# Kernel optimization log

Hardware: AMD Instinct MI355X
Metric: run time of the kernel (lower is better)

## Reference

```python
import jax, jax.numpy as jnp
import numpy as np

# 5-point Laplacian stencil (OIHW), scaled by 1/h^2 = N^2 at each level
FIXED = jnp.array([[[[0.0, 1.0, 0.0], [1.0, -4.0, 1.0], [0.0, 1.0, 0.0]]]], dtype=jnp.float32)
# flex_cycle schedule: depth-2 V-cycle, weighted Jacobi (smoother==1) everywhere
INTERGRID = [-1, -1, 0, 1, 1]
WEIGHT = [0.8, 0.8, 0.8, 0.8, 0.8]
N_GRID = 4096


def _conv(x, k, stride=1):
    return jax.lax.conv_general_dilated(x, k, (stride, stride), 'VALID',
                                        dimension_numbers=('NCHW', 'OIHW', 'NCHW'))


def _pad1(x):
    return jnp.pad(x, ((0, 0), (0, 0), (1, 1), (1, 1)))


def _apply_A(u):
    # F.conv2d(u, N^2 * stencil, padding=0) then zero-pad back to full size
    n = u.shape[-1]
    return _pad1(_conv(u, float(n * n) * FIXED))


def _jacobi(u, f, omega):
    # trainable_weight == 0 and trainable_stencil == fixed_stencil, so the
    # torch update collapses to standard weighted Jacobi
    n = u.shape[-1]
    central = -4.0 * float(n * n)
    return u + omega * (f - _apply_A(u)) / central


def _restrict(r, R):
    return _conv(r, R, stride=2)


def _prolong(u, P):
    up = jnp.repeat(jnp.repeat(u, 2, axis=2), 2, axis=3)  # nearest x2
    return _pad1(_conv(up, P))


def _vcycle(f, R, P):
    u = jnp.zeros_like(f)
    us, fs, lvl = [u], [f], 0
    for op, w in zip(INTERGRID, WEIGHT):
        if op == -1:  # smooth, restrict residual
            us[lvl] = _jacobi(us[lvl], fs[lvl], w)
            r = fs[lvl] - _apply_A(us[lvl])
            fs.append(_restrict(r, R))
            us.append(jnp.zeros_like(fs[-1]))
            lvl += 1
        elif op == 1:  # prolongate + correct, then smooth
            us[lvl - 1] = us[lvl - 1] + _prolong(us[lvl], P)
            lvl -= 1
            us[lvl] = _jacobi(us[lvl], fs[lvl], w)
        else:  # smooth in place
            us[lvl] = _jacobi(us[lvl], fs[lvl], w)
    return us[0]


def setup_inputs() -> dict:
    key = jax.random.key(0)
    f = jax.random.normal(key, (1, 1, N_GRID, N_GRID), dtype=jnp.float32)
    R = jnp.full((1, 1, 2, 2), 0.25, dtype=jnp.float32)
    P = jnp.array([[[[0.25, 0.5, 0.25], [0.5, 1.0, 0.5], [0.25, 0.5, 0.25]]]], dtype=jnp.float32)
    return {"f": f, "restriction_stencils": R, "prolongation_stencils": P}


def reference(f, restriction_stencils, prolongation_stencils):
    # forward() sets max_iter=1 and initial residual (u=0) is 1 > tol,
    # so exactly one flex_cycle runs
    u = _vcycle(f, restriction_stencils, prolongation_stencils)
    res = jnp.sum(jnp.abs(f - _apply_A(u))) / jnp.sum(jnp.abs(f))
    return (u, res)
```

## Files before the change

kernel.cpp:

```cpp
#include <hip/hip_runtime.h>

#define N0 4096
#define N1 2048
#define N2 1024

__global__ __launch_bounds__(256, 4) void k_res_restrict(const float* __restrict__ f,
                                                         float* __restrict__ fc,
                                                         int n, int nc) {
    const int tid = threadIdx.x;
    const int tx = tid & 63, ty = tid >> 6;
    const int fy0 = blockIdx.y * 16, fx0 = blockIdx.x * 256;
    const bool laneL = (tx == 0), laneR = (tx == 63);
    const bool edge = (blockIdx.x == 0) | (blockIdx.y == 0) |
                      (blockIdx.x == gridDim.x - 1) | (blockIdx.y == gridDim.y - 1);

    float4 o4[6]; float os[6];
    #pragma unroll
    for (int rr = 0; rr < 6; ++rr) {
        int gy = max(0, min(n - 1, fy0 + 4 * ty - 1 + rr));
        const float* rowp = f + (size_t)gy * n;
        o4[rr] = *(const float4*)(rowp + fx0 + 4 * tx);
        if (laneL) os[rr] = rowp[max(0, fx0 - 1)];
        if (laneR) os[rr] = rowp[min(n - 1, fx0 + 256)];
    }
    float fa[6][6];
    #pragma unroll
    for (int rr = 0; rr < 6; ++rr) {
        fa[rr][1] = o4[rr].x; fa[rr][2] = o4[rr].y; fa[rr][3] = o4[rr].z; fa[rr][4] = o4[rr].w;
        fa[rr][0] = __shfl_up(o4[rr].w, 1);
        fa[rr][5] = __shfl_down(o4[rr].x, 1);
        if (laneL) fa[rr][0] = os[rr];
        if (laneR) fa[rr][5] = os[rr];
    }
    float rv[4][4];
    #pragma unroll
    for (int i = 0; i < 4; ++i) {
        #pragma unroll
        for (int j = 0; j < 4; ++j) {
            float c = fa[1 + i][1 + j];
            rv[i][j] = c + 0.2f * (fa[i][1 + j] + fa[2 + i][1 + j] +
                                   fa[1 + i][j] + fa[1 + i][2 + j] - 4.0f * c);
        }
    }
    if (edge) {
        #pragma unroll
        for (int i = 0; i < 4; ++i)
            #pragma unroll
            for (int j = 0; j < 4; ++j) {
                int gy = fy0 + 4 * ty + i, gx = fx0 + 4 * tx + j;
                if (gy == 0 || gy == n - 1 || gx == 0 || gx == n - 1)
                    rv[i][j] = fa[1 + i][1 + j];
            }
    }
    #pragma unroll
    for (int da = 0; da < 2; ++da) {
        float2 o;
        o.x = 0.25f * (rv[2*da][0] + rv[2*da][1] + rv[2*da+1][0] + rv[2*da+1][1]);
        o.y = 0.25f * (rv[2*da][2] + rv[2*da][3] + rv[2*da+1][2] + rv[2*da+1][3]);
        *(float2*)(fc + (size_t)(fy0 / 2 + 2 * ty + da) * nc + (fx0 / 2 + 2 * tx)) = o;
    }
}

template <bool RESID>
__global__ __launch_bounds__(512, 4) void k_smooth_wide(
        const float* __restrict__ f, const float* __restrict__ uc,
        float* __restrict__ u, int n, int m, float cf, float cs,
        double* __restrict__ pT, double* __restrict__ pF) {
    __shared__ __align__(16) float su[RESID ? 18 : 1][260];
    __shared__ double sred[16];
    const int tid = threadIdx.x;
    const int tx = tid & 63, ty = tid >> 6;
    const int bx0 = blockIdx.x * 256, by0 = blockIdx.y * 16;
    const int Y  = by0 + 2 * ty;
    const int A0 = by0 >> 1;
    const int A  = A0 + ty;
    const int C  = (bx0 >> 1) + 2 * tx;
    const bool laneL = (tx == 0), laneR = (tx == 63);
    const bool edge = (blockIdx.x == 0) | (blockIdx.y == 0) |
                      (blockIdx.x == gridDim.x - 1) | (blockIdx.y == gridDim.y - 1);

    float4 f4[4]; float fs[4];
    #pragma unroll
    for (int r = 0; r < 4; ++r) {
        int gy = max(0, min(n - 1, Y - 1 + r));
        const float* rowp = f + (size_t)gy * n;
        f4[r] = *(const float4*)(rowp + bx0 + 4 * tx);
        if (laneL) fs[r] = rowp[max(0, bx0 - 1)];
        if (laneR) fs[r] = rowp[min(n - 1, bx0 + 256)];
    }
    float2 c2[3]; float csd[3];
    #pragma unroll
    for (int i = 0; i < 3; ++i) {
        int ga = max(0, min(m - 1, A - 1 + i));
        const float* cp = uc + (size_t)ga * m;
        c2[i] = *(const float2*)(cp + C);
        if (laneL) csd[i] = cp[max(0, C - 1)];
        if (laneR) csd[i] = cp[min(m - 1, C + 2)];
    }
    float4 fH4 = make_float4(0.f, 0.f, 0.f, 0.f); float fHs = 0.f;
    float2 cH2 = make_float2(0.f, 0.f);            float cHs = 0.f;
    float fsd2[2] = {0.f, 0.f}; float csd2[3] = {0.f, 0.f, 0.f};
    if (RESID) {
        if (ty == 0) {
            const float* rowp = f + (size_t)max(0, by0 - 2) * n;
            fH4 = *(const float4*)(rowp + bx0 + 4 * tx);
            if (laneL) fHs = rowp[max(0, bx0 - 1)];
            if (laneR) fHs = rowp[min(n - 1, bx0 + 256)];
            const float* cp = uc + (size_t)max(0, A0 - 2) * m;
            cH2 = *(const float2*)(cp + C);
            if (laneL) cHs = cp[max(0, C - 1)];
            if (laneR) cHs = cp[min(m - 1, C + 2)];
        }
        if (ty == 7) {
            const float* rowp = f + (size_t)min(n - 1, by0 + 17) * n;
            fH4 = *(const float4*)(rowp + bx0 + 4 * tx);
            if (laneL) fHs = rowp[max(0, bx0 - 1)];
            if (laneR) fHs = rowp[min(n - 1, bx0 + 256)];
            const float* cp = uc + (size_t)min(m - 1, A0 + 9) * m;
            cH2 = *(const float2*)(cp + C);
            if (laneL) cHs = cp[max(0, C - 1)];
            if (laneR) cHs = cp[min(m - 1, C + 2)];
        }
        if (laneL) {
            #pragma unroll
            for (int i = 0; i < 3; ++i) {
                int ga = max(0, min(m - 1, A - 1 + i));
                csd2[i] = uc[(size_t)ga * m + max(0, C - 2)];
            }
            #pragma unroll
            for (int k = 0; k < 2; ++k)
                fsd2[k] = f[(size_t)(Y + k) * n + max(0, bx0 - 2)];
        }
        if (laneR) {
            #pragma unroll
            for (int i = 0; i < 3; ++i) {
                int ga = max(0, min(m - 1, A - 1 + i));
                csd2[i] = uc[(size_t)ga * m + min(m - 1, C + 3)];
            }
            #pragma unroll
            for (int k = 0; k < 2; ++k)
                fsd2[k] = f[(size_t)(Y + k) * n + min(n - 1, bx0 + 257)];
        }
    }

    float fr[4][6];
    #pragma unroll
    for (int r = 0; r < 4; ++r) {
        fr[r][1] = f4[r].x; fr[r][2] = f4[r].y; fr[r][3] = f4[r].z; fr[r][4] = f4[r].w;
        fr[r][0] = __shfl_up(f4[r].w, 1);
        fr[r][5] = __shfl_down(f4[r].x, 1);
        if (laneL) fr[r][0] = fs[r];
        if (laneR) fr[r][5] = fs[r];
    }
    float cu[3][4];
    #pragma unroll
    for (int i = 0; i < 3; ++i) {
        float l  = __shfl_up(c2[i].y, 1);
        float rg = __shfl_down(c2[i].x, 1);
        if (laneL) l  = csd[i];
        if (laneR) rg = csd[i];
        cu[i][0] = cs * l; cu[i][1] = cs * c2[i].x; cu[i][2] = cs * c2[i].y; cu[i][3] = cs * rg;
    }
    float h[3][6];
    #pragma unroll
    for (int i = 0; i < 3; ++i) {
        h[i][0] = 1.5f * cu[i][0] + 0.5f * cu[i][1];
        h[i][1] = 0.5f * cu[i][0] + 1.5f * cu[i][1];
        h[i][2] = 1.5f * cu[i][1] + 0.5f * cu[i][2];
        h[i][3] = 0.5f * cu[i][1] + 1.5f * cu[i][2];
        h[i][4] = 1.5f * cu[i][2] + 0.5f * cu[i][3];
        h[i][5] = 0.5f * cu[i][2] + 1.5f * cu[i][3];
    }
    float v[4][6];
    #pragma unroll
    for (int j = 0; j < 6; ++j) {
        v[0][j] = 1.5f * h[0][j] + 0.5f * h[1][j] + cf * fr[0][j];
        v[1][j] = 0.5f * h[0][j] + 1.5f * h[1][j] + cf * fr[1][j];
        v[2][j] = 1.5f * h[1][j] + 0.5f * h[2][j] + cf * fr[2][j];
        v[3][j] = 0.5f * h[1][j] + 1.5f * h[2][j] + cf * fr[3][j];
    }
    if (edge) {
        #pragma unroll
        for (int r = 0; r < 4; ++r)
            #pragma unroll
            for (int j = 0; j < 6; ++j) {
                int gy = Y - 1 + r, gx = bx0 + 4 * tx - 1 + j;
                if (gy == 0 || gy == n - 1 || gx == 0 || gx == n - 1) v[r][j] = cf * fr[r][j];
            }
    }
    float u2[2][4];
    #pragma unroll
    for (int rr = 0; rr < 2; ++rr)
        #pragma unroll
        for (int cc = 0; cc < 4; ++cc) {
            float vc = v[1 + rr][1 + cc];
            u2[rr][cc] = vc + cf * fr[1 + rr][1 + cc]
                       + 0.2f * (v[rr][1 + cc] + v[2 + rr][1 + cc] +
                                 v[1 + rr][cc] + v[1 + rr][2 + cc] - 4.0f * vc);
        }
    if (edge) {
        #pragma unroll
        for (int rr = 0; rr < 2; ++rr)
            #pragma unroll
            for (int cc = 0; cc < 4; ++cc) {
                int gy = Y + rr, gx = bx0 + 4 * tx + cc;
                if (gy == 0 || gy == n - 1 || gx == 0 || gx == n - 1)
                    u2[rr][cc] = v[1 + rr][1 + cc] + cf * fr[1 + rr][1 + cc];
            }
    }
    #pragma unroll
    for (int rr = 0; rr < 2; ++rr)
        *(float4*)(u + (size_t)(Y + rr) * n + (bx0 + 4 * tx)) =
            make_float4(u2[rr][0], u2[rr][1], u2[rr][2], u2[rr][3]);

    if (RESID) {
        if (ty == 0) {
            float l  = __shfl_up(cH2.y, 1);
            float rg = __shfl_down(cH2.x, 1);
            if (laneL) l  = cHs;
            if (laneR) rg = cHs;
            l *= cs; rg *= cs;
            float ox = cs * cH2.x, oy = cs * cH2.y;
            float hm[4] = { 0.5f * l + 1.5f * ox, 1.5f * ox + 0.5f * oy,
                            0.5f * ox + 1.5f * oy, 1.5f * oy + 0.5f * rg };
            float fmv[4] = { fH4.x, fH4.y, fH4.z, fH4.w };
            float vm[4], uHt[4];
            #pragma unroll
            for (int cc = 0; cc < 4; ++cc) vm[cc] = 0.5f * hm[cc] + 1.5f * h[0][1 + cc] + cf * fmv[cc];
            if (edge) {
                #pragma unroll
                for (int cc = 0; cc < 4; ++cc) {
                    int gx = bx0 + 4 * tx + cc;
                    if (gx == 0 || gx == n - 1) vm[cc] = cf * fmv[cc];
                }
            }
            #pragma unroll
            for (int cc = 0; cc < 4; ++cc) {
                float vc = v[0][1 + cc];
                uHt[cc] = vc + cf * fr[0][1 + cc]
                        + 0.2f * (vm[cc] + v[1][1 + cc] + v[0][cc] + v[0][2 + cc] - 4.0f * vc);
            }
            if (edge) {
                #pragma unroll
                for (int cc = 0; cc < 4; ++cc) {
                    int gx = bx0 + 4 * tx + cc;
                    if (gx == 0 || gx == n - 1) uHt[cc] = v[0][1 + cc] + cf * fr[0][1 + cc];
                }
            }
            *(float4*)&su[0][4 * tx] = make_float4(uHt[0], uHt[1], uHt[2], uHt[3]);
        }
        if (ty == 7) {
            float l  = __shfl_up(cH2.y, 1);
            float rg = __shfl_down(cH2.x, 1);
            if (laneL) l  = cHs;
            if (laneR) rg = cHs;
            l *= cs; rg *= cs;
            float ox = cs * cH2.x, oy = cs * cH2.y;
            float hp[4] = { 0.5f * l + 1.5f * ox, 1.5f * ox + 0.5f * oy,
                            0.5f * ox + 1.5f * oy, 1.5f * oy + 0.5f * rg };
            float fpv[4] = { fH4.x, fH4.y, fH4.z, fH4.w };
            float vp[4], uHb[4];
            #pragma unroll
            for (int cc = 0; cc < 4; ++cc) vp[cc] = 1.5f * h[2][1 + cc] + 0.5f * hp[cc] + cf * fpv[cc];
            if (edge) {
                #pragma unroll
                for (int cc = 0; cc < 4; ++cc) {
                    int gx = bx0 + 4 * tx + cc;
                    if (gx == 0 || gx == n - 1) vp[cc] = cf * fpv[cc];
                }
            }
            #pragma unroll
            for (int cc = 0; cc < 4; ++cc) {
                float vc = v[3][1 + cc];
                uHb[cc] = vc + cf * fr[3][1 + cc]
                        + 0.2f * (v[2][1 + cc] + vp[cc] + v[3][cc] + v[3][2 + cc] - 4.0f * vc);
            }
            if (edge) {
                #pragma unroll
                for (int cc = 0; cc < 4; ++cc) {
                    int gx = bx0 + 4 * tx + cc;
                    if (gx == 0 || gx == n - 1) uHb[cc] = v[3][1 + cc] + cf * fr[3][1 + cc];
                }
            }
            *(float4*)&su[17][4 * tx] = make_float4(uHb[0], uHb[1], uHb[2], uHb[3]);
        }
        float uL[2] = {0.f, 0.f}, uR[2] = {0.f, 0.f};
        if (laneL) {
            float hL[3];
            #pragma unroll
            for (int i = 0; i < 3; ++i) hL[i] = 0.5f * cs * csd2[i] + 1.5f * cu[i][0];
            float vL[2] = { 0.5f * hL[0] + 1.5f * hL[1] + cf * fsd2[0],
                            1.5f * hL[1] + 0.5f * hL[2] + cf * fsd2[1] };
            if (edge) {
                #pragma unroll
                for (int k = 0; k < 2; ++k) {
                    int gy = Y + k;
                    if (gy == 0 || gy == n - 1) vL[k] = cf * fsd2[k];
                }
            }
            #pragma unroll
            for (int rr = 0; rr < 2; ++rr) {
                float vc = v[1 + rr][0];
                uL[rr] = vc + cf * fr[1 + rr][0]
                       + 0.2f * (v[rr][0] + v[2 + rr][0] + vL[rr] + v[1 + rr][1] - 4.0f * vc);
                if (edge) {
                    int gy = Y + rr;
                    if (gy == 0 || gy == n - 1) uL[rr] = vc + cf * fr[1 + rr][0];
                }
            }
        }
        if (laneR) {
            float hR[3];
            #pragma unroll
            for (int i = 0; i < 3; ++i) hR[i] = 1.5f * cu[i][3] + 0.5f * cs * csd2[i];
            float vR[2] = { 0.5f * hR[0] + 1.5f * hR[1] + cf * fsd2[0],
                            1.5f * hR[1] + 0.5f * hR[2] + cf * fsd2[1] };
            if (edge) {
                #pragma unroll
                for (int k = 0; k < 2; ++k) {
                    int gy = Y + k;
                    if (gy == 0 || gy == n - 1) vR[k] = cf * fsd2[k];
                }
            }
            #pragma unroll
            for (int rr = 0; rr < 2; ++rr) {
                float vc = v[1 + rr][5];
                uR[rr] = vc + cf * fr[1 + rr][5]
                       + 0.2f * (v[rr][5] + v[2 + rr][5] + v[1 + rr][4] + vR[rr] - 4.0f * vc);
                if (edge) {
                    int gy = Y + rr;
                    if (gy == 0 || gy == n - 1) uR[rr] = vc + cf * fr[1 + rr][5];
                }
            }
        }
        #pragma unroll
        for (int rr = 0; rr < 2; ++rr)
            *(float4*)&su[2 * ty + 1 + rr][4 * tx] =
                make_float4(u2[rr][0], u2[rr][1], u2[rr][2], u2[rr][3]);
        __syncthreads();
        float4 tv = *(const float4*)&su[2 * ty][4 * tx];
        float4 bv = *(const float4*)&su[2 * ty + 3][4 * tx];
        float ta[4] = { tv.x, tv.y, tv.z, tv.w };
        float ba[4] = { bv.x, bv.y, bv.z, bv.w };
        float lft[2], rgt[2];
        lft[0] = __shfl_up(u2[0][3], 1);   lft[1] = __shfl_up(u2[1][3], 1);
        rgt[0] = __shfl_down(u2[0][0], 1); rgt[1] = __shfl_down(u2[1][0], 1);
        if (laneL) { lft[0] = uL[0]; lft[1] = uL[1]; }
        if (laneR) { rgt[0] = uR[0]; rgt[1] = uR[1]; }
        const float n2 = (float)n * (float)n;
        float accT = 0.0f, accF = 0.0f;
        #pragma unroll
        for (int rr = 0; rr < 2; ++rr)
            #pragma unroll
            for (int cc = 0; cc < 4; ++cc) {
                float up = (rr == 0) ? ta[cc] : u2[0][cc];
                float dn = (rr == 1) ? ba[cc] : u2[1][cc];
                float lf = (cc == 0) ? lft[rr] : u2[rr][cc - 1];
                float rt = (cc == 3) ? rgt[rr] : u2[rr][cc + 1];
                float uu = u2[rr][cc];
                float fij = fr[1 + rr][1 + cc];
                float L = up + dn + lf + rt - 4.0f * uu;
                float t = fabsf(fij - n2 * L);
                if (edge) {
                    int gy = Y + rr, gx = bx0 + 4 * tx + cc;
                    if (gy == 0 || gy == n - 1 || gx == 0 || gx == n - 1) t = fabsf(fij);
                }
                accT += t;
                accF += fabsf(fij);
            }
        double vT = (double)accT, vF = (double)accF;
        #pragma unroll
        for (int off = 32; off > 0; off >>= 1) {
            vT += __shfl_down(vT, off);
            vF += __shfl_down(vF, off);
        }
        if (tx == 0) { sred[ty] = vT; sred[8 + ty] = vF; }
        __syncthreads();
        if (tid == 0) {
            double sT = 0.0, sF = 0.0;
            #pragma unroll
            for (int w = 0; w < 8; ++w) { sT += sred[w]; sF += sred[8 + w]; }
            int bid = blockIdx.y * gridDim.x + blockIdx.x;
            pT[bid] = sT;
            pF[bid] = sF;
        }
    }
}

__global__ void k_final(const double* __restrict__ pT, const double* __restrict__ pF,
                        int nb, float* __restrict__ out_res) {
    __shared__ double sT[256], sF[256];
    double tT = 0.0, tF = 0.0;
    for (int i = threadIdx.x; i < nb; i += 256) { tT += pT[i]; tF += pF[i]; }
    sT[threadIdx.x] = tT; sF[threadIdx.x] = tF;
    __syncthreads();
    for (int s = 128; s > 0; s >>= 1) {
        if (threadIdx.x < s) { sT[threadIdx.x] += sT[threadIdx.x + s]; sF[threadIdx.x] += sF[threadIdx.x + s]; }
        __syncthreads();
    }
    if (threadIdx.x == 0) *out_res = (float)(sT[0] / sF[0]);
}

extern "C" void kernel_launch(void* const* d_in, const int* in_sizes, int n_in,
                              void* d_out, int out_size, void* d_ws, size_t ws_size,
                              hipStream_t stream) {
    const float* f0 = (const float*)d_in[0];
    float* u0  = (float*)d_out;
    float* res = u0 + (size_t)N0 * N0;

    char* ws = (char*)d_ws;
    float* f1 = (float*)ws;
    float* u1 = (float*)(ws + (size_t)N1 * N1 * 4);
    float* f2 = (float*)(ws + (size_t)2 * N1 * N1 * 4);
    double* pT = (double*)(ws + (size_t)2 * N1 * N1 * 4 + (size_t)N2 * N2 * 4);
    const int NB = (N0 / 256) * (N0 / 16);
    double* pF = pT + NB;

    const float c0 = -0.2f / ((float)N0 * (float)N0);
    const float c1 = -0.2f / ((float)N1 * (float)N1);
    const float c2 = -0.2f / ((float)N2 * (float)N2);

    k_res_restrict<<<dim3(N0 / 256, N0 / 16), 256, 0, stream>>>(f0, f1, N0, N1);
    k_res_restrict<<<dim3(N1 / 256, N1 / 16), 256, 0, stream>>>(f1, f2, N1, N2);
    k_smooth_wide<false><<<dim3(N1 / 256, N1 / 16), 512, 0, stream>>>(
        f1, f2, u1, N1, N2, c1, c2, nullptr, nullptr);
    k_smooth_wide<true><<<dim3(N0 / 256, N0 / 16), 512, 0, stream>>>(
        f0, u1, u0, N0, N1, c0, 1.0f, pT, pF);
    k_final<<<1, 256, 0, stream>>>(pT, pF, NB, res);
}
```

Baseline: 86.36 us.

## Split residual reduction out of fine-level smoother into separate kernel

Removes the fused residual computation from the fine-level smoothing kernel, which needed halo recomputation, shared memory and barriers. A new standalone kernel re-reads f and the final u to compute the residual sums. This simplifies the smoother and may raise its occupancy, at the cost of an extra full-grid pass over f and u (about 128 MB of traffic at 4096^2) and one more launch. Partial sums inside a block now use float instead of double.

```diff
diff --git a/kernel.cpp b/kernel.cpp
--- a/kernel.cpp
+++ b/kernel.cpp
@@ -61,19 +61,14 @@
     }
 }
 
-template <bool RESID>
-__global__ __launch_bounds__(512, 4) void k_smooth_wide(
+__global__ __launch_bounds__(512) void k_smooth_wide(
         const float* __restrict__ f, const float* __restrict__ uc,
-        float* __restrict__ u, int n, int m, float cf, float cs,
-        double* __restrict__ pT, double* __restrict__ pF) {
-    __shared__ __align__(16) float su[RESID ? 18 : 1][260];
-    __shared__ double sred[16];
+        float* __restrict__ u, int n, int m, float cf, float cs) {
     const int tid = threadIdx.x;
     const int tx = tid & 63, ty = tid >> 6;
     const int bx0 = blockIdx.x * 256, by0 = blockIdx.y * 16;
     const int Y  = by0 + 2 * ty;
-    const int A0 = by0 >> 1;
-    const int A  = A0 + ty;
+    const int A  = (by0 >> 1) + ty;
     const int C  = (bx0 >> 1) + 2 * tx;
     const bool laneL = (tx == 0), laneR = (tx == 63);
     const bool edge = (blockIdx.x == 0) | (blockIdx.y == 0) |
@@ -96,51 +91,6 @@
         c2[i] = *(const float2*)(cp + C);
         if (laneL) csd[i] = cp[max(0, C - 1)];
         if (laneR) csd[i] = cp[min(m - 1, C + 2)];
-    }
-    float4 fH4 = make_float4(0.f, 0.f, 0.f, 0.f); float fHs = 0.f;
-    float2 cH2 = make_float2(0.f, 0.f);            float cHs = 0.f;
-    float fsd2[2] = {0.f, 0.f}; float csd2[3] = {0.f, 0.f, 0.f};
-    if (RESID) {
-        if (ty == 0) {
-            const float* rowp = f + (size_t)max(0, by0 - 2) * n;
-            fH4 = *(const float4*)(rowp + bx0 + 4 * tx);
-            if (laneL) fHs = rowp[max(0, bx0 - 1)];
-            if (laneR) fHs = rowp[min(n - 1, bx0 + 256)];
-            const float* cp = uc + (size_t)max(0, A0 - 2) * m;
-            cH2 = *(const float2*)(cp + C);
-            if (laneL) cHs = cp[max(0, C - 1)];
-            if (laneR) cHs = cp[min(m - 1, C + 2)];
-        }
-        if (ty == 7) {
-            const float* rowp = f + (size_t)min(n - 1, by0 + 17) * n;
-            fH4 = *(const float4*)(rowp + bx0 + 4 * tx);
-            if (laneL) fHs = rowp[max(0, bx0 - 1)];
-            if (laneR) fHs = rowp[min(n - 1, bx0 + 256)];
-            const float* cp = uc + (size_t)min(m - 1, A0 + 9) * m;
-            cH2 = *(const float2*)(cp + C);
-            if (laneL) cHs = cp[max(0, C - 1)];
-            if (laneR) cHs = cp[min(m - 1, C + 2)];
-        }
-        if (laneL) {
-            #pragma unroll
-            for (int i = 0; i < 3; ++i) {
-                int ga = max(0, min(m - 1, A - 1 + i));
-                csd2[i] = uc[(size_t)ga * m + max(0, C - 2)];
-            }
-            #pragma unroll
-            for (int k = 0; k < 2; ++k)
-                fsd2[k] = f[(size_t)(Y + k) * n + max(0, bx0 - 2)];
-        }
-        if (laneR) {
-            #pragma unroll
-            for (int i = 0; i < 3; ++i) {
-                int ga = max(0, min(m - 1, A - 1 + i));
-                csd2[i] = uc[(size_t)ga * m + min(m - 1, C + 3)];
-            }
-            #pragma unroll
-            for (int k = 0; k < 2; ++k)
-                fsd2[k] = f[(size_t)(Y + k) * n + min(n - 1, bx0 + 257)];
-        }
     }
 
     float fr[4][6];
@@ -212,178 +162,74 @@
     for (int rr = 0; rr < 2; ++rr)
         *(float4*)(u + (size_t)(Y + rr) * n + (bx0 + 4 * tx)) =
             make_float4(u2[rr][0], u2[rr][1], u2[rr][2], u2[rr][3]);
-
-    if (RESID) {
-        if (ty == 0) {
-            float l  = __shfl_up(cH2.y, 1);
-            float rg = __shfl_down(cH2.x, 1);
-            if (laneL) l  = cHs;
-            if (laneR) rg = cHs;
-            l *= cs; rg *= cs;
-            float ox = cs * cH2.x, oy = cs * cH2.y;
-            float hm[4] = { 0.5f * l + 1.5f * ox, 1.5f * ox + 0.5f * oy,
-                            0.5f * ox + 1.5f * oy, 1.5f * oy + 0.5f * rg };
-            float fmv[4] = { fH4.x, fH4.y, fH4.z, fH4.w };
-            float vm[4], uHt[4];
-            #pragma unroll
-            for (int cc = 0; cc < 4; ++cc) vm[cc] = 0.5f * hm[cc] + 1.5f * h[0][1 + cc] + cf * fmv[cc];
+}
+
+__global__ __launch_bounds__(256, 4) void k_resid(const float* __restrict__ f,
+                                                  const float* __restrict__ u,
+                                                  double* __restrict__ pT,
+                                                  double* __restrict__ pF, int n) {
+    __shared__ float sredT[4], sredF[4];
+    const int tid = threadIdx.x;
+    const int tx = tid & 63, ty = tid >> 6;
+    const int gy0 = blockIdx.y * 16 + 4 * ty, gx0 = blockIdx.x * 256 + 4 * tx;
+    const bool laneL = (tx == 0), laneR = (tx == 63);
+    const bool edge = (blockIdx.x == 0) | (blockIdx.y == 0) |
+                      (blockIdx.x == gridDim.x - 1) | (blockIdx.y == gridDim.y - 1);
+
+    float4 u4[6]; float us[6];
+    #pragma unroll
+    for (int r = 0; r < 6; ++r) {
+        int gy = max(0, min(n - 1, gy0 - 1 + r));
+        const float* rowp = u + (size_t)gy * n;
+        u4[r] = *(const float4*)(rowp + gx0);
+        if (laneL) us[r] = rowp[max(0, gx0 - 1)];
+        if (laneR) us[r] = rowp[min(n - 1, gx0 + 4)];
+    }
+    float4 f4[4];
+    #pragma unroll
+    for (int r = 0; r < 4; ++r)
+        f4[r] = *(const float4*)(f + (size_t)(gy0 + r) * n + gx0);
+
+    float ua[6][6];
+    #pragma unroll
+    for (int r = 0; r < 6; ++r) {
+        ua[r][1] = u4[r].x; ua[r][2] = u4[r].y; ua[r][3] = u4[r].z; ua[r][4] = u4[r].w;
+        ua[r][0] = __shfl_up(u4[r].w, 1);
+        ua[r][5] = __shfl_down(u4[r].x, 1);
+        if (laneL) ua[r][0] = us[r];
+        if (laneR) ua[r][5] = us[r];
+    }
+
+    const float n2 = (float)n * (float)n;
+    float accT = 0.0f, accF = 0.0f;
+    #pragma unroll
+    for (int k = 0; k < 4; ++k) {
+        float fv[4] = { f4[k].x, f4[k].y, f4[k].z, f4[k].w };
+        #pragma unroll
+        for (int j = 0; j < 4; ++j) {
+            float uu = ua[k + 1][j + 1];
+            float L = ua[k][j + 1] + ua[k + 2][j + 1] +
+                      ua[k + 1][j] + ua[k + 1][j + 2] - 4.0f * uu;
+            float t = fabsf(fv[j] - n2 * L);
             if (edge) {
-                #pragma unroll
-                for (int cc = 0; cc < 4; ++cc) {
-                    int gx = bx0 + 4 * tx + cc;
-                    if (gx == 0 || gx == n - 1) vm[cc] = cf * fmv[cc];
-                }
-            }
-            #pragma unroll
-            for (int cc = 0; cc < 4; ++cc) {
-                float vc = v[0][1 + cc];
-                uHt[cc] = vc + cf * fr[0][1 + cc]
-                        + 0.2f * (vm[cc] + v[1][1 + cc] + v[0][cc] + v[0][2 + cc] - 4.0f * vc);
-            }
-            if (edge) {
-                #pragma unroll
-                for (int cc = 0; cc < 4; ++cc) {
-                    int gx = bx0 + 4 * tx + cc;
-                    if (gx == 0 || gx == n - 1) uHt[cc] = v[0][1 + cc] + cf * fr[0][1 + cc];
-                }
-            }
-            *(float4*)&su[0][4 * tx] = make_float4(uHt[0], uHt[1], uHt[2], uHt[3]);
+                int gy = gy0 + k, gx = gx0 + j;
+                if (gy == 0 || gy == n - 1 || gx == 0 || gx == n - 1) t = fabsf(fv[j]);
+            }
+            accT += t;
+            accF += fabsf(fv[j]);
         }
-        if (ty == 7) {
-            float l  = __shfl_up(cH2.y, 1);
-            float rg = __shfl_down(cH2.x, 1);
-            if (laneL) l  = cHs;
-            if (laneR) rg = cHs;
-            l *= cs; rg *= cs;
-            float ox = cs * cH2.x, oy = cs * cH2.y;
-            float hp[4] = { 0.5f * l + 1.5f * ox, 1.5f * ox + 0.5f * oy,
-                            0.5f * ox + 1.5f * oy, 1.5f * oy + 0.5f * rg };
-            float fpv[4] = { fH4.x, fH4.y, fH4.z, fH4.w };
-            float vp[4], uHb[4];
-            #pragma unroll
-            for (int cc = 0; cc < 4; ++cc) vp[cc] = 1.5f * h[2][1 + cc] + 0.5f * hp[cc] + cf * fpv[cc];
-            if (edge) {
-                #pragma unroll
-                for (int cc = 0; cc < 4; ++cc) {
-                    int gx = bx0 + 4 * tx + cc;
-                    if (gx == 0 || gx == n - 1) vp[cc] = cf * fpv[cc];
-                }
-            }
-            #pragma unroll
-            for (int cc = 0; cc < 4; ++cc) {
-                float vc = v[3][1 + cc];
-                uHb[cc] = vc + cf * fr[3][1 + cc]
-                        + 0.2f * (v[2][1 + cc] + vp[cc] + v[3][cc] + v[3][2 + cc] - 4.0f * vc);
-            }
-            if (edge) {
-                #pragma unroll
-                for (int cc = 0; cc < 4; ++cc) {
-                    int gx = bx0 + 4 * tx + cc;
-                    if (gx == 0 || gx == n - 1) uHb[cc] = v[3][1 + cc] + cf * fr[3][1 + cc];
-                }
-            }
-            *(float4*)&su[17][4 * tx] = make_float4(uHb[0], uHb[1], uHb[2], uHb[3]);
-        }
-        float uL[2] = {0.f, 0.f}, uR[2] = {0.f, 0.f};
-        if (laneL) {
-            float hL[3];
-            #pragma unroll
-            for (int i = 0; i < 3; ++i) hL[i] = 0.5f * cs * csd2[i] + 1.5f * cu[i][0];
-            float vL[2] = { 0.5f * hL[0] + 1.5f * hL[1] + cf * fsd2[0],
-                            1.5f * hL[1] + 0.5f * hL[2] + cf * fsd2[1] };
-            if (edge) {
-                #pragma unroll
-                for (int k = 0; k < 2; ++k) {
-                    int gy = Y + k;
-                    if (gy == 0 || gy == n - 1) vL[k] = cf * fsd2[k];
-                }
-            }
-            #pragma unroll
-            for (int rr = 0; rr < 2; ++rr) {
-                float vc = v[1 + rr][0];
-                uL[rr] = vc + cf * fr[1 + rr][0]
-                       + 0.2f * (v[rr][0] + v[2 + rr][0] + vL[rr] + v[1 + rr][1] - 4.0f * vc);
-                if (edge) {
-                    int gy = Y + rr;
-                    if (gy == 0 || gy == n - 1) uL[rr] = vc + cf * fr[1 + rr][0];
-                }
-            }
-        }
-        if (laneR) {
-            float hR[3];
-            #pragma unroll
-            for (int i = 0; i < 3; ++i) hR[i] = 1.5f * cu[i][3] + 0.5f * cs * csd2[i];
-            float vR[2] = { 0.5f * hR[0] + 1.5f * hR[1] + cf * fsd2[0],
-                            1.5f * hR[1] + 0.5f * hR[2] + cf * fsd2[1] };
-            if (edge) {
-                #pragma unroll
-                for (int k = 0; k < 2; ++k) {
-                    int gy = Y + k;
-                    if (gy == 0 || gy == n - 1) vR[k] = cf * fsd2[k];
-                }
-            }
-            #pragma unroll
-            for (int rr = 0; rr < 2; ++rr) {
-                float vc = v[1 + rr][5];
-                uR[rr] = vc + cf * fr[1 + rr][5]
-                       + 0.2f * (v[rr][5] + v[2 + rr][5] + v[1 + rr][4] + vR[rr] - 4.0f * vc);
-                if (edge) {
-                    int gy = Y + rr;
-                    if (gy == 0 || gy == n - 1) uR[rr] = vc + cf * fr[1 + rr][5];
-                }
-            }
-        }
-        #pragma unroll
-        for (int rr = 0; rr < 2; ++rr)
-            *(float4*)&su[2 * ty + 1 + rr][4 * tx] =
-                make_float4(u2[rr][0], u2[rr][1], u2[rr][2], u2[rr][3]);
-        __syncthreads();
-        float4 tv = *(const float4*)&su[2 * ty][4 * tx];
-        float4 bv = *(const float4*)&su[2 * ty + 3][4 * tx];
-        float ta[4] = { tv.x, tv.y, tv.z, tv.w };
-        float ba[4] = { bv.x, bv.y, bv.z, bv.w };
-        float lft[2], rgt[2];
-        lft[0] = __shfl_up(u2[0][3], 1);   lft[1] = __shfl_up(u2[1][3], 1);
-        rgt[0] = __shfl_down(u2[0][0], 1); rgt[1] = __shfl_down(u2[1][0], 1);
-        if (laneL) { lft[0] = uL[0]; lft[1] = uL[1]; }
-        if (laneR) { rgt[0] = uR[0]; rgt[1] = uR[1]; }
-        const float n2 = (float)n * (float)n;
-        float accT = 0.0f, accF = 0.0f;
-        #pragma unroll
-        for (int rr = 0; rr < 2; ++rr)
-            #pragma unroll
-            for (int cc = 0; cc < 4; ++cc) {
-                float up = (rr == 0) ? ta[cc] : u2[0][cc];
-                float dn = (rr == 1) ? ba[cc] : u2[1][cc];
-                float lf = (cc == 0) ? lft[rr] : u2[rr][cc - 1];
-                float rt = (cc == 3) ? rgt[rr] : u2[rr][cc + 1];
-                float uu = u2[rr][cc];
-                float fij = fr[1 + rr][1 + cc];
-                float L = up + dn + lf + rt - 4.0f * uu;
-                float t = fabsf(fij - n2 * L);
-                if (edge) {
-                    int gy = Y + rr, gx = bx0 + 4 * tx + cc;
-                    if (gy == 0 || gy == n - 1 || gx == 0 || gx == n - 1) t = fabsf(fij);
-                }
-                accT += t;
-                accF += fabsf(fij);
-            }
-        double vT = (double)accT, vF = (double)accF;
-        #pragma unroll
-        for (int off = 32; off > 0; off >>= 1) {
-            vT += __shfl_down(vT, off);
-            vF += __shfl_down(vF, off);
-        }
-        if (tx == 0) { sred[ty] = vT; sred[8 + ty] = vF; }
-        __syncthreads();
-        if (tid == 0) {
-            double sT = 0.0, sF = 0.0;
-            #pragma unroll
-            for (int w = 0; w < 8; ++w) { sT += sred[w]; sF += sred[8 + w]; }
-            int bid = blockIdx.y * gridDim.x + blockIdx.x;
-            pT[bid] = sT;
-            pF[bid] = sF;
-        }
+    }
+    #pragma unroll
+    for (int off = 32; off > 0; off >>= 1) {
+        accT += __shfl_down(accT, off);
+        accF += __shfl_down(accF, off);
+    }
+    if (tx == 0) { sredT[ty] = accT; sredF[ty] = accF; }
+    __syncthreads();
+    if (tid == 0) {
+        int bid = blockIdx.y * gridDim.x + blockIdx.x;
+        pT[bid] = (double)sredT[0] + sredT[1] + sredT[2] + sredT[3];
+        pF[bid] = (double)sredF[0] + sredF[1] + sredF[2] + sredF[3];
     }
 }
 
@@ -422,9 +268,10 @@
 
     k_res_restrict<<<dim3(N0 / 256, N0 / 16), 256, 0, stream>>>(f0, f1, N0, N1);
     k_res_restrict<<<dim3(N1 / 256, N1 / 16), 256, 0, stream>>>(f1, f2, N1, N2);
-    k_smooth_wide<false><<<dim3(N1 / 256, N1 / 16), 512, 0, stream>>>(
-        f1, f2, u1, N1, N2, c1, c2, nullptr, nullptr);
-    k_smooth_wide<true><<<dim3(N0 / 256, N0 / 16), 512, 0, stream>>>(
-        f0, u1, u0, N0, N1, c0, 1.0f, pT, pF);
+    k_smooth_wide<<<dim3(N1 / 256, N1 / 16), 512, 0, stream>>>(
+        f1, f2, u1, N1, N2, c1, c2);
+    k_smooth_wide<<<dim3(N0 / 256, N0 / 16), 512, 0, stream>>>(
+        f0, u1, u0, N0, N1, c0, 1.0f);
+    k_resid<<<dim3(N0 / 256, N0 / 16), 256, 0, stream>>>(f0, u0, pT, pF, N0);
     k_final<<<1, 256, 0, stream>>>(pT, pF, NB, res);
 }
```

New measurement: 90.81 us. 5.2% more time.
